# Performance work log

Hardware: AMD Instinct MI355X
Metric: run time of the kernel (lower is better)

## Reference

```python
import jax, jax.numpy as jnp
import numpy as np

B, T, I, H = 8192, 658, 7, 1
D1, D2, D3 = 1024, 512, 128


def setup_inputs() -> dict:
    key = jax.random.key(0)
    ks = jax.random.split(key, 14)
    return {
        "x": jax.random.normal(ks[0], (B, T, I), dtype=jnp.float32),
        "h0": jax.random.uniform(ks[1], (1, B, H), dtype=jnp.float32),
        "W_ih": jax.random.normal(ks[2], (H, I), dtype=jnp.float32) * 0.3,
        "W_hh": jax.random.normal(ks[3], (H, H), dtype=jnp.float32) * 0.3,
        "b_ih": jax.random.normal(ks[4], (H,), dtype=jnp.float32) * 0.1,
        "b_hh": jax.random.normal(ks[5], (H,), dtype=jnp.float32) * 0.1,
        "w1": jax.random.normal(ks[6], (D1, T), dtype=jnp.float32) * 0.03,
        "b1": jax.random.normal(ks[7], (D1,), dtype=jnp.float32) * 0.01,
        "w2": jax.random.normal(ks[8], (D2, D1), dtype=jnp.float32) * 0.03,
        "b2": jax.random.normal(ks[9], (D2,), dtype=jnp.float32) * 0.01,
        "w3": jax.random.normal(ks[10], (D3, D2), dtype=jnp.float32) * 0.03,
        "b3": jax.random.normal(ks[11], (D3,), dtype=jnp.float32) * 0.01,
        "w4": jax.random.normal(ks[12], (T, D3), dtype=jnp.float32) * 0.03,
        "b4": jax.random.normal(ks[13], (T,), dtype=jnp.float32) * 0.01,
    }


def _forward(x, h0, W_ih, W_hh, b_ih, b_hh, w1, b1, w2, b2, w3, b3, w4, b4):
    # Precompute input projection for all timesteps: [T, B, H]
    xw = jnp.einsum("bti,hi->tbh", x, W_ih) + b_ih

    def step(h, xw_t):  # h: [B, H]
        h_new = jnp.tanh(xw_t + h @ W_hh.T + b_hh)
        return h_new, h_new

    h_last, hs = jax.lax.scan(step, h0[0], xw)  # hs: [T, B, H]
    out = jnp.transpose(hs, (1, 0, 2)).reshape(-1, T)  # [B, T] (view(-1, seq))

    out = jax.nn.relu(out @ w1.T + b1)
    out = jax.nn.relu(out @ w2.T + b2)
    out = jax.nn.relu(out @ w3.T + b3)
    out = out @ w4.T + b4
    return out, h_last[None]  # hidden: [1, B, H]


def reference(x, h0, W_ih, W_hh, b_ih, b_hh, w1, b1, w2, b2, w3, b3, w4, b4):
    return _forward(x, h0, W_ih, W_hh, b_ih, b_hh, w1, b1, w2, b2, w3, b3, w4, b4)
```

## Files before the change

kernel.cpp:

```cpp
#include <hip/hip_runtime.h>
#include <hip/hip_bf16.h>
#include <stdint.h>
#include <stddef.h>

#define B_  8192
#define T_  658
#define I_  7
#define TP  672
#define D1_ 1024
#define D2_ 512
#define D3_ 128
#define NP4 768

#define NB  64
#define CT  32
#define NCH 21

#define XWBLKS 21504
#define CVBLKS 5376

typedef __bf16 bf16x8 __attribute__((ext_vector_type(8)));
typedef float  floatx4 __attribute__((ext_vector_type(4)));

__device__ __forceinline__ void gload_lds16(const void* g, void* l) {
    __builtin_amdgcn_global_load_lds(
        (const __attribute__((address_space(1))) void*)g,
        (__attribute__((address_space(3))) void*)l, 16, 0, 0);
}

__device__ __forceinline__ unsigned int pack_bf16x2(float a, float b) {
    unsigned int ua = __float_as_uint(a);
    unsigned int ub = __float_as_uint(b);
    ua += 0x7fffu + ((ua >> 16) & 1u);
    ub += 0x7fffu + ((ub >> 16) & 1u);
    return (ua >> 16) | (ub & 0xffff0000u);
}

__device__ __forceinline__ float bf16lo(unsigned int u) { return __uint_as_float(u << 16); }
__device__ __forceinline__ float bf16hi(unsigned int u) { return __uint_as_float(u & 0xffff0000u); }

__global__ void xw_conv_kernel(const float* __restrict__ x,
                               const float* __restrict__ Wih,
                               const float* __restrict__ bih,
                               __bf16* __restrict__ xwb,
                               const float* __restrict__ w1, const float* __restrict__ w2,
                               const float* __restrict__ w3, const float* __restrict__ w4,
                               __bf16* __restrict__ w1b, __bf16* __restrict__ w2b,
                               __bf16* __restrict__ w3b, __bf16* __restrict__ w4b) {
    if (blockIdx.x < XWBLKS) {
        const int i = blockIdx.x * 256 + threadIdx.x;
        const int b = i / TP, t = i - b * TP;
        float s = 0.0f;
        if (t < T_) {
            const float* xp = x + ((size_t)b * T_ + t) * I_;
            s = bih[0];
#pragma unroll
            for (int j = 0; j < I_; ++j) s = fmaf(xp[j], Wih[j], s);
        }
        xwb[i] = (__bf16)s;
        return;
    }
    int i = (blockIdx.x - XWBLKS) * 256 + threadIdx.x;
    if (i < D1_ * TP) {
        int r = i / TP, c = i - r * TP;
        w1b[i] = (__bf16)(c < T_ ? w1[r * T_ + c] : 0.0f);
        return;
    }
    i -= D1_ * TP;
    if (i < D2_ * D1_) { w2b[i] = (__bf16)w2[i]; return; }
    i -= D2_ * D1_;
    if (i < D3_ * D2_) { w3b[i] = (__bf16)w3[i]; return; }
    i -= D3_ * D2_;
    {
        int r = i / D3_, c = i - r * D3_;
        w4b[i] = (__bf16)(r < T_ ? w4[r * D3_ + c] : 0.0f);
    }
}

__global__ __launch_bounds__(64) void scan_kernel(
    const __bf16* __restrict__ xwb, const float* __restrict__ h0,
    const float* __restrict__ Whh, const float* __restrict__ bhh,
    __bf16* __restrict__ A0, float* __restrict__ hlast) {
    __shared__ float        lds_x[CT * (NB + 1)];
    __shared__ unsigned int lds_o[NB * 17];

    const int tid = threadIdx.x;
    const int b0 = blockIdx.x * NB;
    const float whh = Whh[0], bh = bhh[0];
    const float C2L = 2.8853900817779268f;
    const float whhc = whh * C2L;
    float h = h0[b0 + tid];

    uint4 pf[4];
    unsigned int res[CT / 2];

#pragma unroll
    for (int l = 0; l < 4; ++l) {
        const int idx = l * NB + tid;
        const int bl = idx >> 2, q = idx & 3;
        pf[l] = *(const uint4*)(xwb + (size_t)(b0 + bl) * TP + q * 8);
    }

    for (int c = 0; c < NCH; ++c) {
        const int t0 = c * CT;
        __syncthreads();
#pragma unroll
        for (int l = 0; l < 4; ++l) {
            const int idx = l * NB + tid;
            const int bl = idx >> 2, q = idx & 3;
            const uint4 v = pf[l];
            lds_x[(q * 8 + 0) * (NB + 1) + bl] = bf16lo(v.x);
            lds_x[(q * 8 + 1) * (NB + 1) + bl] = bf16hi(v.x);
            lds_x[(q * 8 + 2) * (NB + 1) + bl] = bf16lo(v.y);
            lds_x[(q * 8 + 3) * (NB + 1) + bl] = bf16hi(v.y);
            lds_x[(q * 8 + 4) * (NB + 1) + bl] = bf16lo(v.z);
            lds_x[(q * 8 + 5) * (NB + 1) + bl] = bf16hi(v.z);
            lds_x[(q * 8 + 6) * (NB + 1) + bl] = bf16lo(v.w);
            lds_x[(q * 8 + 7) * (NB + 1) + bl] = bf16hi(v.w);
        }
        if (c > 0) {
#pragma unroll
            for (int j = 0; j < 16; ++j) lds_o[tid * 17 + j] = res[j];
        }
        __syncthreads();
        if (c > 0) {
            const int tprev = t0 - CT;
#pragma unroll
            for (int l = 0; l < 4; ++l) {
                const int idx = l * NB + tid;
                const int bl = idx >> 2, q = idx & 3;
                uint4 v;
                v.x = lds_o[bl * 17 + q * 4 + 0];
                v.y = lds_o[bl * 17 + q * 4 + 1];
                v.z = lds_o[bl * 17 + q * 4 + 2];
                v.w = lds_o[bl * 17 + q * 4 + 3];
                *(uint4*)(A0 + (size_t)(b0 + bl) * TP + tprev + q * 8) = v;
            }
        }
        if (c + 1 < NCH) {
            const int tn = t0 + CT;
#pragma unroll
            for (int l = 0; l < 4; ++l) {
                const int idx = l * NB + tid;
                const int bl = idx >> 2, q = idx & 3;
                pf[l] = *(const uint4*)(xwb + (size_t)(b0 + bl) * TP + tn + q * 8);
            }
        }
        if (c < NCH - 1) {
#pragma unroll
            for (int k = 0; k < CT; k += 2) {
                float xv0 = lds_x[k * (NB + 1) + tid];
                float xv1 = lds_x[(k + 1) * (NB + 1) + tid];
                float e0 = __builtin_amdgcn_exp2f(fmaf(h, whhc, (xv0 + bh) * C2L));
                h = fmaf(-2.0f, __builtin_amdgcn_rcpf(e0 + 1.0f), 1.0f);
                float r0 = h;
                float e1 = __builtin_amdgcn_exp2f(fmaf(h, whhc, (xv1 + bh) * C2L));
                h = fmaf(-2.0f, __builtin_amdgcn_rcpf(e1 + 1.0f), 1.0f);
                res[k >> 1] = pack_bf16x2(r0, h);
            }
        } else {
            const int nval = T_ - t0;
#pragma unroll
            for (int k = 0; k < CT; k += 2) {
                float r0 = 0.0f, r1 = 0.0f;
                if (k < nval) {
                    float xv0 = lds_x[k * (NB + 1) + tid];
                    float e0 = __builtin_amdgcn_exp2f(fmaf(h, whhc, (xv0 + bh) * C2L));
                    h = fmaf(-2.0f, __builtin_amdgcn_rcpf(e0 + 1.0f), 1.0f);
                    r0 = h;
                }
                if (k + 1 < nval) {
                    float xv1 = lds_x[(k + 1) * (NB + 1) + tid];
                    float e1 = __builtin_amdgcn_exp2f(fmaf(h, whhc, (xv1 + bh) * C2L));
                    h = fmaf(-2.0f, __builtin_amdgcn_rcpf(e1 + 1.0f), 1.0f);
                    r1 = h;
                }
                res[k >> 1] = pack_bf16x2(r0, r1);
            }
        }
    }
    __syncthreads();
#pragma unroll
    for (int j = 0; j < 16; ++j) lds_o[tid * 17 + j] = res[j];
    __syncthreads();
    {
        const int tprev = TP - CT;
#pragma unroll
        for (int l = 0; l < 4; ++l) {
            const int idx = l * NB + tid;
            const int bl = idx >> 2, q = idx & 3;
            uint4 v;
            v.x = lds_o[bl * 17 + q * 4 + 0];
            v.y = lds_o[bl * 17 + q * 4 + 1];
            v.z = lds_o[bl * 17 + q * 4 + 2];
            v.w = lds_o[bl * 17 + q * 4 + 3];
            *(uint4*)(A0 + (size_t)(b0 + bl) * TP + tprev + q * 8) = v;
        }
    }
    hlast[b0 + tid] = h;
}

template<int BM, int BN>
__global__ __launch_bounds__(256, 4) void gemm_bt(
    const __bf16* __restrict__ A, const __bf16* __restrict__ W,
    const float* __restrict__ bias, __bf16* __restrict__ outb,
    float* __restrict__ outf, int K, int Npad, int Nreal, int relu) {
    constexpr int MI = BM / 32;
    constexpr int NJ = BN / 32;
    constexpr int nA = BM / 64;
    constexpr int nB = BN / 64;
    __shared__ __align__(16) __bf16 As[BM * 32];
    __shared__ __align__(16) __bf16 Bs[BN * 32];

    const int tid = threadIdx.x;
    const int m0 = blockIdx.x * BM, n0 = blockIdx.y * BN;
    const int lane = tid & 63, wave = tid >> 6;
    const int wm = (wave & 1) * (BM / 2), wn = (wave >> 1) * (BN / 2);
    const int quad = lane >> 4, l16 = lane & 15;

    const int eoff = tid * 8;
    const int rowS = eoff >> 5;
    const int colS = eoff & 31;
    const __bf16* gaa[nA];
    const __bf16* gbb[nB];
    __bf16* laa[nA];
    __bf16* lbb[nB];
#pragma unroll
    for (int c = 0; c < nA; ++c) {
        gaa[c] = A + (size_t)(m0 + rowS + c * 64) * K + colS;
        laa[c] = As + c * 2048 + (tid & 192) * 8;
    }
#pragma unroll
    for (int c = 0; c < nB; ++c) {
        gbb[c] = W + (size_t)(n0 + rowS + c * 64) * K + colS;
        lbb[c] = Bs + c * 2048 + (tid & 192) * 8;
    }

    floatx4 acc[MI][NJ] = {};

    for (int k0 = 0; k0 < K; k0 += 32) {
#pragma unroll
        for (int c = 0; c < nA; ++c) gload_lds16(gaa[c] + k0, laa[c]);
#pragma unroll
        for (int c = 0; c < nB; ++c) gload_lds16(gbb[c] + k0, lbb[c]);
        __syncthreads();

        bf16x8 af[MI], bg[NJ];
#pragma unroll
        for (int i = 0; i < MI; ++i)
            af[i] = *(const bf16x8*)(As + (wm + i * 16 + l16) * 32 + quad * 8);
#pragma unroll
        for (int j = 0; j < NJ; ++j)
            bg[j] = *(const bf16x8*)(Bs + (wn + j * 16 + l16) * 32 + quad * 8);
#pragma unroll
        for (int i = 0; i < MI; ++i)
#pragma unroll
            for (int j = 0; j < NJ; ++j)
                acc[i][j] = __builtin_amdgcn_mfma_f32_16x16x32_bf16(af[i], bg[j], acc[i][j], 0, 0, 0);
        __syncthreads();
    }

#pragma unroll
    for (int j = 0; j < NJ; ++j) {
        const int n = n0 + wn + j * 16 + l16;
        const float bv = (n < Nreal) ? bias[n] : 0.0f;
#pragma unroll
        for (int i = 0; i < MI; ++i) {
#pragma unroll
            for (int r = 0; r < 4; ++r) {
                const int m = m0 + wm + i * 16 + quad * 4 + r;
                float v = acc[i][j][r] + bv;
                if (relu) v = fmaxf(v, 0.0f);
                if (outb) {
                    outb[(size_t)m * Npad + n] = (__bf16)v;
                } else if (n < Nreal) {
                    outf[(size_t)m * Nreal + n] = v;
                }
            }
        }
    }
}

extern "C" void kernel_launch(void* const* d_in, const int* in_sizes, int n_in,
                              void* d_out, int out_size, void* d_ws, size_t ws_size,
                              hipStream_t stream) {
    const float* x   = (const float*)d_in[0];
    const float* h0  = (const float*)d_in[1];
    const float* Wih = (const float*)d_in[2];
    const float* Whh = (const float*)d_in[3];
    const float* bih = (const float*)d_in[4];
    const float* bhh = (const float*)d_in[5];
    const float* w1  = (const float*)d_in[6];
    const float* b1  = (const float*)d_in[7];
    const float* w2  = (const float*)d_in[8];
    const float* b2  = (const float*)d_in[9];
    const float* w3  = (const float*)d_in[10];
    const float* b3  = (const float*)d_in[11];
    const float* w4  = (const float*)d_in[12];
    const float* b4  = (const float*)d_in[13];
    float* out = (float*)d_out;
    char* ws = (char*)d_ws;

    __bf16* w1b = (__bf16*)(ws + 0);
    __bf16* w2b = (__bf16*)(ws + 1376256);
    __bf16* w3b = (__bf16*)(ws + 2424832);
    __bf16* w4b = (__bf16*)(ws + 2555904);
    __bf16* A0  = (__bf16*)(ws + 2752512);
    __bf16* A1  = (__bf16*)(ws + 13762560);
    __bf16* A2  = (__bf16*)(ws + 30539776);
    __bf16* A3  = (__bf16*)(ws + 38928384);
    __bf16* xwb = (__bf16*)(ws + 13762560);

    xw_conv_kernel<<<XWBLKS + CVBLKS, 256, 0, stream>>>(
        x, Wih, bih, xwb, w1, w2, w3, w4, w1b, w2b, w3b, w4b);
    scan_kernel<<<128, 64, 0, stream>>>(xwb, h0, Whh, bhh, A0, out + (size_t)B_ * T_);

    gemm_bt<64,128><<<dim3(128, 8), 256, 0, stream>>>(A0, w1b, b1, A1, nullptr, TP,  D1_, D1_, 1);
    gemm_bt<64,64> <<<dim3(128, 8), 256, 0, stream>>>(A1, w2b, b2, A2, nullptr, D1_, D2_, D2_, 1);
    gemm_bt<64,64> <<<dim3(128, 2), 256, 0, stream>>>(A2, w3b, b3, A3, nullptr, D2_, D3_, D3_, 1);
    gemm_bt<64,128><<<dim3(128, 6), 256, 0, stream>>>(A3, w4b, b4, nullptr, out, D3_, NP4, T_, 0);
}
```

Before: 333.7 us.

## Double-buffer LDS tiles in bf16 GEMM and widen second layer tile

The GEMM kernel now keeps two LDS buffers and prefetches the next K-slice while running MFMAs on the current one, which removes one barrier per iteration and hides global-load latency. The second MLP layer also switches from a 64x64 tile to a 64x128 tile, halving its grid. The cost is double the LDS per block, which may lower occupancy, and fewer blocks for layer 2.

```diff
diff --git a/kernel.cpp b/kernel.cpp
--- a/kernel.cpp
+++ b/kernel.cpp
@@ -209,8 +209,8 @@
     constexpr int NJ = BN / 32;
     constexpr int nA = BM / 64;
     constexpr int nB = BN / 64;
-    __shared__ __align__(16) __bf16 As[BM * 32];
-    __shared__ __align__(16) __bf16 Bs[BN * 32];
+    __shared__ __align__(16) __bf16 As[2][BM * 32];
+    __shared__ __align__(16) __bf16 Bs[2][BN * 32];
 
     const int tid = threadIdx.x;
     const int m0 = blockIdx.x * BM, n0 = blockIdx.y * BN;
@@ -223,41 +223,42 @@
     const int colS = eoff & 31;
     const __bf16* gaa[nA];
     const __bf16* gbb[nB];
-    __bf16* laa[nA];
-    __bf16* lbb[nB];
-#pragma unroll
-    for (int c = 0; c < nA; ++c) {
-        gaa[c] = A + (size_t)(m0 + rowS + c * 64) * K + colS;
-        laa[c] = As + c * 2048 + (tid & 192) * 8;
-    }
-#pragma unroll
-    for (int c = 0; c < nB; ++c) {
-        gbb[c] = W + (size_t)(n0 + rowS + c * 64) * K + colS;
-        lbb[c] = Bs + c * 2048 + (tid & 192) * 8;
-    }
+#pragma unroll
+    for (int c = 0; c < nA; ++c) gaa[c] = A + (size_t)(m0 + rowS + c * 64) * K + colS;
+#pragma unroll
+    for (int c = 0; c < nB; ++c) gbb[c] = W + (size_t)(n0 + rowS + c * 64) * K + colS;
+    const int ldsoff = (tid & 192) * 8;
 
     floatx4 acc[MI][NJ] = {};
-
-    for (int k0 = 0; k0 < K; k0 += 32) {
-#pragma unroll
-        for (int c = 0; c < nA; ++c) gload_lds16(gaa[c] + k0, laa[c]);
-#pragma unroll
-        for (int c = 0; c < nB; ++c) gload_lds16(gbb[c] + k0, lbb[c]);
+    const int nIter = K >> 5;
+
+#pragma unroll
+    for (int c = 0; c < nA; ++c) gload_lds16(gaa[c], &As[0][c * 2048 + ldsoff]);
+#pragma unroll
+    for (int c = 0; c < nB; ++c) gload_lds16(gbb[c], &Bs[0][c * 2048 + ldsoff]);
+
+    for (int it = 0; it < nIter; ++it) {
+        const int cur = it & 1, nxt = cur ^ 1;
         __syncthreads();
-
+        if (it + 1 < nIter) {
+            const int k0 = (it + 1) * 32;
+#pragma unroll
+            for (int c = 0; c < nA; ++c) gload_lds16(gaa[c] + k0, &As[nxt][c * 2048 + ldsoff]);
+#pragma unroll
+            for (int c = 0; c < nB; ++c) gload_lds16(gbb[c] + k0, &Bs[nxt][c * 2048 + ldsoff]);
+        }
         bf16x8 af[MI], bg[NJ];
 #pragma unroll
         for (int i = 0; i < MI; ++i)
-            af[i] = *(const bf16x8*)(As + (wm + i * 16 + l16) * 32 + quad * 8);
+            af[i] = *(const bf16x8*)(&As[cur][(wm + i * 16 + l16) * 32 + quad * 8]);
 #pragma unroll
         for (int j = 0; j < NJ; ++j)
-            bg[j] = *(const bf16x8*)(Bs + (wn + j * 16 + l16) * 32 + quad * 8);
+            bg[j] = *(const bf16x8*)(&Bs[cur][(wn + j * 16 + l16) * 32 + quad * 8]);
 #pragma unroll
         for (int i = 0; i < MI; ++i)
 #pragma unroll
             for (int j = 0; j < NJ; ++j)
                 acc[i][j] = __builtin_amdgcn_mfma_f32_16x16x32_bf16(af[i], bg[j], acc[i][j], 0, 0, 0);
-        __syncthreads();
     }
 
 #pragma unroll
@@ -316,7 +317,7 @@
     scan_kernel<<<128, 64, 0, stream>>>(xwb, h0, Whh, bhh, A0, out + (size_t)B_ * T_);
 
     gemm_bt<64,128><<<dim3(128, 8), 256, 0, stream>>>(A0, w1b, b1, A1, nullptr, TP,  D1_, D1_, 1);
-    gemm_bt<64,64> <<<dim3(128, 8), 256, 0, stream>>>(A1, w2b, b2, A2, nullptr, D1_, D2_, D2_, 1);
+    gemm_bt<64,128><<<dim3(128, 4), 256, 0, stream>>>(A1, w2b, b2, A2, nullptr, D1_, D2_, D2_, 1);
     gemm_bt<64,64> <<<dim3(128, 2), 256, 0, stream>>>(A2, w3b, b3, A3, nullptr, D2_, D3_, D3_, 1);
     gemm_bt<64,128><<<dim3(128, 6), 256, 0, stream>>>(A3, w4b, b4, nullptr, out, D3_, NP4, T_, 0);
 }
```

Result: no change. 334.7 us (+0.3%).
